# Performance work log

Hardware: AMD Instinct MI355X
Metric: run time of the kernel (lower is better)

The kernel has to match this reference:

```python
import jax, jax.numpy as jnp
import numpy as np

L, D, H = 4096, 1024, 16
HEAD_DIM = D // H
SCALE = 1.0 / float(np.sqrt(HEAD_DIM))


def setup_inputs() -> dict:
    key = jax.random.key(0)
    kq, kk, kv = jax.random.split(key, 3)
    Q = jax.random.normal(kq, (L, D), dtype=jnp.float32)
    K = jax.random.normal(kk, (L, D), dtype=jnp.float32)
    V = jax.random.normal(kv, (L, D), dtype=jnp.float32)
    return {"Q": Q, "K": K, "V": V}


def reference(Q, K, V):
    # [L, D] -> [H, L, head_dim]; contiguous head slices of D (matches the
    # original per-head slicing Q[:, h*hd:(h+1)*hd]).
    q = Q.reshape(L, H, HEAD_DIM).transpose(1, 0, 2)
    k = K.reshape(L, H, HEAD_DIM).transpose(1, 0, 2)
    v = V.reshape(L, H, HEAD_DIM).transpose(1, 0, 2)
    # scores: [H, L, L]
    scores = jnp.einsum('hqd,hkd->hqk', q, k) * SCALE
    probs = jax.nn.softmax(scores, axis=-1)
    out = jnp.einsum('hqk,hkd->hqd', probs, v)  # [H, L, head_dim]
    # merge heads back to [L, D]
    return out.transpose(1, 0, 2).reshape(L, D)
```

## Files before the change

### kernel.cpp

```cpp
#include <hip/hip_runtime.h>
#include <hip/hip_bf16.h>

#define SEQ_L 4096
#define DIM_D 1024
#define NHEAD 16
#define HDIM  64
#define QBLK  64
#define KVB   128
#define NTILE (SEQ_L / KVB)
#define QSCALE 0.180336880f
#define NSHIFT -17.3123405f

typedef __attribute__((ext_vector_type(8))) short bf16x8;
typedef __attribute__((ext_vector_type(4))) short bf16x4;
typedef __attribute__((ext_vector_type(4))) float f32x4;

__device__ __forceinline__ short f2bf(float f) {
    union { float f; unsigned u; } x; x.f = f;
    unsigned r = x.u + 0x7fffu + ((x.u >> 16) & 1u);
    return (short)(r >> 16);
}

__device__ __forceinline__ float fast_exp2(float x) {
#if __has_builtin(__builtin_amdgcn_exp2f)
    return __builtin_amdgcn_exp2f(x);
#else
    return exp2f(x);
#endif
}

__device__ __forceinline__ bf16x4 pk4t(float p0, float p1, float p2, float p3) {
#if __has_builtin(__builtin_amdgcn_perm)
    union { float f; unsigned u; } a0, a1, a2, a3;
    a0.f = p0; a1.f = p1; a2.f = p2; a3.f = p3;
    union { unsigned u[2]; bf16x4 v; } cv;
    cv.u[0] = __builtin_amdgcn_perm(a1.u, a0.u, 0x07060302u);
    cv.u[1] = __builtin_amdgcn_perm(a3.u, a2.u, 0x07060302u);
    return cv.v;
#else
    const bf16x4 r = { f2bf(p0), f2bf(p1), f2bf(p2), f2bf(p3) };
    return r;
#endif
}

__device__ __forceinline__ void gl16(const void* g, void* l) {
    __builtin_amdgcn_global_load_lds(
        (const __attribute__((address_space(1))) unsigned int*)g,
        (__attribute__((address_space(3))) unsigned int*)l, 16, 0, 0);
}

__global__ void cvt_qk(const float* __restrict__ Q, const float* __restrict__ K,
                       short* __restrict__ Qb, short* __restrict__ Kb) {
    const size_t n8 = (size_t)SEQ_L * DIM_D / 8;
    size_t j = (size_t)blockIdx.x * blockDim.x + threadIdx.x;
    const float* src; short* dst; float sc;
    if (j < n8) { src = Q; dst = Qb; sc = QSCALE; }
    else        { src = K; dst = Kb; sc = 1.0f; j -= n8; }
    const float4 a = *(const float4*)(src + j*8);
    const float4 b = *(const float4*)(src + j*8 + 4);
    bf16x8 v;
    v[0]=f2bf(a.x*sc); v[1]=f2bf(a.y*sc); v[2]=f2bf(a.z*sc); v[3]=f2bf(a.w*sc);
    v[4]=f2bf(b.x*sc); v[5]=f2bf(b.y*sc); v[6]=f2bf(b.z*sc); v[7]=f2bf(b.w*sc);
    *(bf16x8*)(dst + j*8) = v;
}

__global__ void cvt_vT(const float* __restrict__ V, short* __restrict__ VT) {
    __shared__ short tile[64][136];
    const int t = threadIdx.x;
    const int kv0 = blockIdx.x * 128;
    const int h = blockIdx.y;
#pragma unroll
    for (int i = 0; i < 8; ++i) {
        const int idx = i*256 + t;
        const int row = idx >> 4, cg = idx & 15;
        const float4 v = *(const float4*)(V + (size_t)(kv0+row)*DIM_D + h*HDIM + cg*4);
        tile[cg*4+0][row] = f2bf(v.x);
        tile[cg*4+1][row] = f2bf(v.y);
        tile[cg*4+2][row] = f2bf(v.z);
        tile[cg*4+3][row] = f2bf(v.w);
    }
    __syncthreads();
#pragma unroll
    for (int i = 0; i < 4; ++i) {
        const int idx = i*256 + t;
        const int d = idx >> 4, cg = idx & 15;
        *(bf16x8*)(VT + ((size_t)h*HDIM + d)*SEQ_L + kv0 + cg*8) = *(const bf16x8*)&tile[d][cg*8];
    }
}

__launch_bounds__(256, 2)
__global__ void attn_split(const short* __restrict__ Qb, const short* __restrict__ Kb,
                           const short* __restrict__ VT, float* __restrict__ Og) {
    __shared__ union {
        struct { short K[KVB*64]; short V[8192]; } s;
        struct { float Ob0[64*68]; float Ob1[64*68]; float ls[4][64]; } r;
    } u;

    const int t = threadIdx.x;
    const int w = t >> 6, lane = t & 63;
    const int g = lane >> 4, c = lane & 15;
    const int c7 = c & 7;

    const int flat = blockIdx.x;
    const int f2 = (flat & 7) * 128 + (flat >> 3);
    const int h = f2 >> 6, qi = f2 & 63;
    const int qb = qi * QBLK, hc = h * HDIM;

    bf16x8 qa[4][2];
#pragma unroll
    for (int qt = 0; qt < 4; ++qt)
#pragma unroll
        for (int ds = 0; ds < 2; ++ds)
            qa[qt][ds] = *(const bf16x8*)&Qb[(size_t)(qb + qt*16 + c) * DIM_D + hc + ds*32 + g*8];

    f32x4 o[4][4], os[4];
#pragma unroll
    for (int qt = 0; qt < 4; ++qt) {
        os[qt] = (f32x4){0.f,0.f,0.f,0.f};
#pragma unroll
        for (int db = 0; db < 4; ++db) o[qt][db] = (f32x4){0.f,0.f,0.f,0.f};
    }
    const short oneb = (short)0x3F80;
    const bf16x8 ones8 = { oneb, oneb, oneb, oneb, oneb, oneb, oneb, oneb };

    int koff[4], vgo[4]; unsigned kdst[4], vdst[4];
#pragma unroll
    for (int i = 0; i < 4; ++i) {
        const int s = lane >> 3;
        const int jj = i*8 + s;
        const int kvp = ((jj & 15) >> 2)*8 + (jj >> 4)*4 + (jj & 3);
        koff[i] = (w*32 + kvp) * DIM_D + (((lane & 7) ^ s) * 8);
        kdst[i] = (unsigned)(w*32 + i*8) * 128;
        vgo[i]  = (i*16 + c) * SEQ_L + w*32 + g*8;
        vdst[i] = (unsigned)(w*4096 + i*1024);
    }

    const short* Kh  = Kb + hc;
    const short* VTh = VT + (size_t)h * HDIM * SEQ_L;

#pragma unroll
    for (int i = 0; i < 4; ++i) {
        gl16(Kh + koff[i], (char*)u.s.K + kdst[i]);
        gl16(VTh + vgo[i], (char*)u.s.V + vdst[i]);
    }

    for (int tile = 0; tile < NTILE; ++tile) {
        asm volatile("s_waitcnt vmcnt(0)" ::: "memory");
        __builtin_amdgcn_sched_barrier(0);

        bf16x8 kf[2][2];
#pragma unroll
        for (int ktl = 0; ktl < 2; ++ktl)
#pragma unroll
            for (int ds = 0; ds < 2; ++ds)
                kf[ktl][ds] = *(const bf16x8*)&u.s.K[(w*32 + ktl*16 + c)*64 + (((ds*4 + g) ^ c7) * 8)];

        bf16x8 vv8[4];
#pragma unroll
        for (int db = 0; db < 4; ++db)
            vv8[db] = *(const bf16x8*)&u.s.V[w*2048 + db*512 + (g*16 + c)*8];

        asm volatile("s_waitcnt lgkmcnt(0)" ::: "memory");
        __builtin_amdgcn_sched_barrier(0);

        if (tile + 1 < NTILE) {
            const short* Kt = Kh + (size_t)(tile + 1) * KVB * DIM_D;
            const short* Vt = VTh + (tile + 1) * KVB;
#pragma unroll
            for (int i = 0; i < 4; ++i) {
                gl16(Kt + koff[i], (char*)u.s.K + kdst[i]);
                gl16(Vt + vgo[i], (char*)u.s.V + vdst[i]);
            }
        }

        __builtin_amdgcn_s_setprio(1);
#pragma unroll
        for (int qt = 0; qt < 4; ++qt) {
            f32x4 a0 = (f32x4){NSHIFT, NSHIFT, NSHIFT, NSHIFT};
            f32x4 a1 = (f32x4){NSHIFT, NSHIFT, NSHIFT, NSHIFT};
            a0 = __builtin_amdgcn_mfma_f32_16x16x32_bf16(kf[0][0], qa[qt][0], a0, 0, 0, 0);
            a0 = __builtin_amdgcn_mfma_f32_16x16x32_bf16(kf[0][1], qa[qt][1], a0, 0, 0, 0);
            a1 = __builtin_amdgcn_mfma_f32_16x16x32_bf16(kf[1][0], qa[qt][0], a1, 0, 0, 0);
            a1 = __builtin_amdgcn_mfma_f32_16x16x32_bf16(kf[1][1], qa[qt][1], a1, 0, 0, 0);

            const float p00 = fast_exp2(a0[0]), p01 = fast_exp2(a0[1]);
            const float p02 = fast_exp2(a0[2]), p03 = fast_exp2(a0[3]);
            const float p10 = fast_exp2(a1[0]), p11 = fast_exp2(a1[1]);
            const float p12 = fast_exp2(a1[2]), p13 = fast_exp2(a1[3]);
            const bf16x4 pl = pk4t(p00, p01, p02, p03);
            const bf16x4 ph = pk4t(p10, p11, p12, p13);
            const bf16x8 pb8 = __builtin_shufflevector(pl, ph, 0, 1, 2, 3, 4, 5, 6, 7);

            os[qt] = __builtin_amdgcn_mfma_f32_16x16x32_bf16(ones8, pb8, os[qt], 0, 0, 0);
#pragma unroll
            for (int db = 0; db < 4; ++db)
                o[qt][db] = __builtin_amdgcn_mfma_f32_16x16x32_bf16(vv8[db], pb8, o[qt][db], 0, 0, 0);
        }
        __builtin_amdgcn_s_setprio(0);
    }

    __syncthreads();
    if (lane < 16) {
#pragma unroll
        for (int qt = 0; qt < 4; ++qt) u.r.ls[w][qt*16 + c] = os[qt][0];
    }
    if (w == 0) {
#pragma unroll
        for (int qt = 0; qt < 4; ++qt)
#pragma unroll
            for (int db = 0; db < 4; ++db)
                *(f32x4*)&u.r.Ob0[(qt*16 + c)*68 + db*16 + 4*g] = o[qt][db];
    } else if (w == 1) {
#pragma unroll
        for (int qt = 0; qt < 4; ++qt)
#pragma unroll
            for (int db = 0; db < 4; ++db)
                *(f32x4*)&u.r.Ob1[(qt*16 + c)*68 + db*16 + 4*g] = o[qt][db];
    }
    __syncthreads();
    if (w == 2) {
#pragma unroll
        for (int qt = 0; qt < 4; ++qt)
#pragma unroll
            for (int db = 0; db < 4; ++db) {
                f32x4* p = (f32x4*)&u.r.Ob0[(qt*16 + c)*68 + db*16 + 4*g];
                f32x4 s = *p;
#pragma unroll
                for (int r = 0; r < 4; ++r) s[r] += o[qt][db][r];
                *p = s;
            }
    } else if (w == 3) {
#pragma unroll
        for (int qt = 0; qt < 4; ++qt)
#pragma unroll
            for (int db = 0; db < 4; ++db) {
                f32x4* p = (f32x4*)&u.r.Ob1[(qt*16 + c)*68 + db*16 + 4*g];
                f32x4 s = *p;
#pragma unroll
                for (int r = 0; r < 4; ++r) s[r] += o[qt][db][r];
                *p = s;
            }
    }
    __syncthreads();

    {
        const int row = w*16 + (lane >> 2);
        const int cq = lane & 3;
        const float lt = u.r.ls[0][row] + u.r.ls[1][row] + u.r.ls[2][row] + u.r.ls[3][row];
        const float inv = 1.0f / lt;
        float* op = Og + (size_t)(qb + row) * DIM_D + hc + cq*16;
#pragma unroll
        for (int i = 0; i < 4; ++i) {
            float4 v;
            v.x = (u.r.Ob0[row*68 + cq*16 + i*4 + 0] + u.r.Ob1[row*68 + cq*16 + i*4 + 0]) * inv;
            v.y = (u.r.Ob0[row*68 + cq*16 + i*4 + 1] + u.r.Ob1[row*68 + cq*16 + i*4 + 1]) * inv;
            v.z = (u.r.Ob0[row*68 + cq*16 + i*4 + 2] + u.r.Ob1[row*68 + cq*16 + i*4 + 2]) * inv;
            v.w = (u.r.Ob0[row*68 + cq*16 + i*4 + 3] + u.r.Ob1[row*68 + cq*16 + i*4 + 3]) * inv;
            *(float4*)(op + i*4) = v;
        }
    }
}

#define LDKF 72
__global__ void attn_fwd_fallback(const float* __restrict__ Qg, const float* __restrict__ Kg,
                                  const float* __restrict__ Vg, float* __restrict__ Og) {
    __shared__ short Klds[64 * LDKF];
    __shared__ short Vt[HDIM * LDKF];
    __shared__ short Plds[4 * 16 * LDKF];

    const int t = threadIdx.x;
    const int w = t >> 6, lane = t & 63;
    const int g = lane >> 4, c = lane & 15;
    const int qb = blockIdx.x * 64;
    const int h = blockIdx.y, hc = h * HDIM;

    bf16x8 qa[2];
    {
        const int qrow = qb + w * 16 + c;
        const float* qp = Qg + (size_t)qrow * DIM_D + hc + g * 8;
#pragma unroll
        for (int db = 0; db < 2; ++db) {
            bf16x8 a2;
#pragma unroll
            for (int j = 0; j < 8; ++j) a2[j] = f2bf(qp[db * 32 + j] * 0.125f);
            qa[db] = a2;
        }
    }
    float m[4], lsum[4];
    f32x4 o[4];
#pragma unroll
    for (int r = 0; r < 4; ++r) { m[r] = -1e30f; lsum[r] = 0.f; }
#pragma unroll
    for (int db = 0; db < 4; ++db) o[db] = (f32x4){0.f,0.f,0.f,0.f};
    const int tr = t >> 4, tc = t & 15;

    for (int kv0 = 0; kv0 < SEQ_L; kv0 += 64) {
#pragma unroll
        for (int i = 0; i < 4; ++i) {
            const int kv = tr + i * 16;
            const float4 kf4 = *(const float4*)(Kg + (size_t)(kv0 + kv) * DIM_D + hc + tc * 4);
            short4 ks; ks.x = f2bf(kf4.x); ks.y = f2bf(kf4.y); ks.z = f2bf(kf4.z); ks.w = f2bf(kf4.w);
            *(short4*)&Klds[kv * LDKF + tc * 4] = ks;
            const float4 vf4 = *(const float4*)(Vg + (size_t)(kv0 + kv) * DIM_D + hc + tc * 4);
            Vt[(tc*4+0) * LDKF + kv] = f2bf(vf4.x);
            Vt[(tc*4+1) * LDKF + kv] = f2bf(vf4.y);
            Vt[(tc*4+2) * LDKF + kv] = f2bf(vf4.z);
            Vt[(tc*4+3) * LDKF + kv] = f2bf(vf4.w);
        }
        __syncthreads();
        f32x4 acc[4];
#pragma unroll
        for (int kt = 0; kt < 4; ++kt) {
            f32x4 a2 = (f32x4){0.f,0.f,0.f,0.f};
#pragma unroll
            for (int db = 0; db < 2; ++db) {
                bf16x8 kb = *(const bf16x8*)&Klds[(kt*16 + c) * LDKF + db*32 + g*8];
                a2 = __builtin_amdgcn_mfma_f32_16x16x32_bf16(qa[db], kb, a2, 0, 0, 0);
            }
            acc[kt] = a2;
        }
        float tmax[4];
#pragma unroll
        for (int r = 0; r < 4; ++r)
            tmax[r] = fmaxf(fmaxf(acc[0][r], acc[1][r]), fmaxf(acc[2][r], acc[3][r]));
#pragma unroll
        for (int mask = 1; mask < 16; mask <<= 1)
#pragma unroll
            for (int r = 0; r < 4; ++r) tmax[r] = fmaxf(tmax[r], __shfl_xor(tmax[r], mask));
        float alpha[4], ps[4];
#pragma unroll
        for (int r = 0; r < 4; ++r) {
            const float mn = fmaxf(m[r], tmax[r]);
            alpha[r] = __expf(m[r] - mn); m[r] = mn; ps[r] = 0.f;
        }
#pragma unroll
        for (int kt = 0; kt < 4; ++kt)
#pragma unroll
            for (int r = 0; r < 4; ++r) {
                const float p = __expf(acc[kt][r] - m[r]);
                ps[r] += p;
                Plds[(w*16 + g*4 + r) * LDKF + kt*16 + c] = f2bf(p);
            }
#pragma unroll
        for (int mask = 1; mask < 16; mask <<= 1)
#pragma unroll
            for (int r = 0; r < 4; ++r) ps[r] += __shfl_xor(ps[r], mask);
#pragma unroll
        for (int r = 0; r < 4; ++r) lsum[r] = lsum[r] * alpha[r] + ps[r];
#pragma unroll
        for (int db = 0; db < 4; ++db)
#pragma unroll
            for (int r = 0; r < 4; ++r) o[db][r] *= alpha[r];
#pragma unroll
        for (int db = 0; db < 4; ++db)
#pragma unroll
            for (int kb = 0; kb < 2; ++kb) {
                bf16x8 pa = *(const bf16x8*)&Plds[(w*16 + c) * LDKF + kb*32 + g*8];
                bf16x8 vb = *(const bf16x8*)&Vt[(db*16 + c) * LDKF + kb*32 + g*8];
                o[db] = __builtin_amdgcn_mfma_f32_16x16x32_bf16(pa, vb, o[db], 0, 0, 0);
            }
        __syncthreads();
    }
#pragma unroll
    for (int r = 0; r < 4; ++r) {
        const float inv = 1.0f / lsum[r];
        const int qrow = qb + w*16 + g*4 + r;
        float* op = Og + (size_t)qrow * DIM_D + hc;
#pragma unroll
        for (int db = 0; db < 4; ++db) op[db*16 + c] = o[db][r] * inv;
    }
}

extern "C" void kernel_launch(void* const* d_in, const int* in_sizes, int n_in,
                              void* d_out, int out_size, void* d_ws, size_t ws_size,
                              hipStream_t stream) {
    (void)in_sizes; (void)n_in; (void)out_size;
    const float* Q = (const float*)d_in[0];
    const float* K = (const float*)d_in[1];
    const float* V = (const float*)d_in[2];
    float* O = (float*)d_out;

    const size_t n = (size_t)SEQ_L * DIM_D;
    const size_t need = 3 * n * sizeof(short);
    if (ws_size >= need) {
        short* Qb = (short*)d_ws;
        short* Kb = Qb + n;
        short* VT = Qb + 2 * n;
        hipLaunchKernelGGL(cvt_qk, dim3(2 * n / 8 / 256), dim3(256), 0, stream, Q, K, Qb, Kb);
        hipLaunchKernelGGL(cvt_vT, dim3(SEQ_L / 128, NHEAD), dim3(256), 0, stream, V, VT);
        hipLaunchKernelGGL(attn_split, dim3(1024), dim3(256), 0, stream, Qb, Kb, VT, O);
    } else {
        hipLaunchKernelGGL(attn_fwd_fallback, dim3(SEQ_L / 64, NHEAD), dim3(256), 0, stream, Q, K, V, O);
    }
}
```

Measured before the change: 106.4 us.

## Halve query block to 32 rows, raise occupancy, compute row sums with VALU

Shrinks the per-block query tile from 64 to 32 rows, which doubles the grid to 2048 blocks and raises the launch-bounds occupancy target from 2 to 3 blocks per CU. It also replaces the ones-vector MFMA used for softmax denominators with scalar adds plus cross-lane shuffles, and remaps the epilogue so each thread writes 8 output floats. The goal is more parallelism and latency hiding plus fewer MFMA issues per tile. The cost is that each K/V tile now serves half as many queries, which doubles global K/V traffic and the staging work per query.

```diff
diff --git a/kernel.cpp b/kernel.cpp
--- a/kernel.cpp
+++ b/kernel.cpp
@@ -5,7 +5,7 @@
 #define DIM_D 1024
 #define NHEAD 16
 #define HDIM  64
-#define QBLK  64
+#define QBLK  32
 #define KVB   128
 #define NTILE (SEQ_L / KVB)
 #define QSCALE 0.180336880f
@@ -88,12 +88,12 @@
     }
 }
 
-__launch_bounds__(256, 2)
+__launch_bounds__(256, 3)
 __global__ void attn_split(const short* __restrict__ Qb, const short* __restrict__ Kb,
                            const short* __restrict__ VT, float* __restrict__ Og) {
     __shared__ union {
         struct { short K[KVB*64]; short V[8192]; } s;
-        struct { float Ob0[64*68]; float Ob1[64*68]; float ls[4][64]; } r;
+        struct { float Ob0[32*68]; float Ob1[32*68]; float ls[4][32]; } r;
     } u;
 
     const int t = threadIdx.x;
@@ -102,26 +102,25 @@
     const int c7 = c & 7;
 
     const int flat = blockIdx.x;
-    const int f2 = (flat & 7) * 128 + (flat >> 3);
-    const int h = f2 >> 6, qi = f2 & 63;
+    const int f2 = (flat & 7) * 256 + (flat >> 3);
+    const int h = f2 >> 7, qi = f2 & 127;
     const int qb = qi * QBLK, hc = h * HDIM;
 
-    bf16x8 qa[4][2];
-#pragma unroll
-    for (int qt = 0; qt < 4; ++qt)
+    bf16x8 qa[2][2];
+#pragma unroll
+    for (int qt = 0; qt < 2; ++qt)
 #pragma unroll
         for (int ds = 0; ds < 2; ++ds)
             qa[qt][ds] = *(const bf16x8*)&Qb[(size_t)(qb + qt*16 + c) * DIM_D + hc + ds*32 + g*8];
 
-    f32x4 o[4][4], os[4];
-#pragma unroll
-    for (int qt = 0; qt < 4; ++qt) {
-        os[qt] = (f32x4){0.f,0.f,0.f,0.f};
+    f32x4 o[2][4];
+    float psum[2];
+#pragma unroll
+    for (int qt = 0; qt < 2; ++qt) {
+        psum[qt] = 0.f;
 #pragma unroll
         for (int db = 0; db < 4; ++db) o[qt][db] = (f32x4){0.f,0.f,0.f,0.f};
     }
-    const short oneb = (short)0x3F80;
-    const bf16x8 ones8 = { oneb, oneb, oneb, oneb, oneb, oneb, oneb, oneb };
 
     int koff[4], vgo[4]; unsigned kdst[4], vdst[4];
 #pragma unroll
@@ -175,7 +174,7 @@
 
         __builtin_amdgcn_s_setprio(1);
 #pragma unroll
-        for (int qt = 0; qt < 4; ++qt) {
+        for (int qt = 0; qt < 2; ++qt) {
             f32x4 a0 = (f32x4){NSHIFT, NSHIFT, NSHIFT, NSHIFT};
             f32x4 a1 = (f32x4){NSHIFT, NSHIFT, NSHIFT, NSHIFT};
             a0 = __builtin_amdgcn_mfma_f32_16x16x32_bf16(kf[0][0], qa[qt][0], a0, 0, 0, 0);
@@ -187,11 +186,11 @@
             const float p02 = fast_exp2(a0[2]), p03 = fast_exp2(a0[3]);
             const float p10 = fast_exp2(a1[0]), p11 = fast_exp2(a1[1]);
             const float p12 = fast_exp2(a1[2]), p13 = fast_exp2(a1[3]);
+            psum[qt] += ((p00 + p01) + (p02 + p03)) + ((p10 + p11) + (p12 + p13));
             const bf16x4 pl = pk4t(p00, p01, p02, p03);
             const bf16x4 ph = pk4t(p10, p11, p12, p13);
             const bf16x8 pb8 = __builtin_shufflevector(pl, ph, 0, 1, 2, 3, 4, 5, 6, 7);
 
-            os[qt] = __builtin_amdgcn_mfma_f32_16x16x32_bf16(ones8, pb8, os[qt], 0, 0, 0);
 #pragma unroll
             for (int db = 0; db < 4; ++db)
                 o[qt][db] = __builtin_amdgcn_mfma_f32_16x16x32_bf16(vv8[db], pb8, o[qt][db], 0, 0, 0);
@@ -199,20 +198,25 @@
         __builtin_amdgcn_s_setprio(0);
     }
 
+#pragma unroll
+    for (int qt = 0; qt < 2; ++qt) {
+        psum[qt] += __shfl_xor(psum[qt], 16);
+        psum[qt] += __shfl_xor(psum[qt], 32);
+    }
     __syncthreads();
     if (lane < 16) {
-#pragma unroll
-        for (int qt = 0; qt < 4; ++qt) u.r.ls[w][qt*16 + c] = os[qt][0];
+        u.r.ls[w][c]      = psum[0];
+        u.r.ls[w][16 + c] = psum[1];
     }
     if (w == 0) {
 #pragma unroll
-        for (int qt = 0; qt < 4; ++qt)
+        for (int qt = 0; qt < 2; ++qt)
 #pragma unroll
             for (int db = 0; db < 4; ++db)
                 *(f32x4*)&u.r.Ob0[(qt*16 + c)*68 + db*16 + 4*g] = o[qt][db];
     } else if (w == 1) {
 #pragma unroll
-        for (int qt = 0; qt < 4; ++qt)
+        for (int qt = 0; qt < 2; ++qt)
 #pragma unroll
             for (int db = 0; db < 4; ++db)
                 *(f32x4*)&u.r.Ob1[(qt*16 + c)*68 + db*16 + 4*g] = o[qt][db];
@@ -220,7 +224,7 @@
     __syncthreads();
     if (w == 2) {
 #pragma unroll
-        for (int qt = 0; qt < 4; ++qt)
+        for (int qt = 0; qt < 2; ++qt)
 #pragma unroll
             for (int db = 0; db < 4; ++db) {
                 f32x4* p = (f32x4*)&u.r.Ob0[(qt*16 + c)*68 + db*16 + 4*g];
@@ -231,7 +235,7 @@
             }
     } else if (w == 3) {
 #pragma unroll
-        for (int qt = 0; qt < 4; ++qt)
+        for (int qt = 0; qt < 2; ++qt)
 #pragma unroll
             for (int db = 0; db < 4; ++db) {
                 f32x4* p = (f32x4*)&u.r.Ob1[(qt*16 + c)*68 + db*16 + 4*g];
@@ -244,20 +248,23 @@
     __syncthreads();
 
     {
-        const int row = w*16 + (lane >> 2);
-        const int cq = lane & 3;
+        const int row = t >> 3;
+        const int j8 = t & 7;
         const float lt = u.r.ls[0][row] + u.r.ls[1][row] + u.r.ls[2][row] + u.r.ls[3][row];
         const float inv = 1.0f / lt;
-        float* op = Og + (size_t)(qb + row) * DIM_D + hc + cq*16;
-#pragma unroll
-        for (int i = 0; i < 4; ++i) {
-            float4 v;
-            v.x = (u.r.Ob0[row*68 + cq*16 + i*4 + 0] + u.r.Ob1[row*68 + cq*16 + i*4 + 0]) * inv;
-            v.y = (u.r.Ob0[row*68 + cq*16 + i*4 + 1] + u.r.Ob1[row*68 + cq*16 + i*4 + 1]) * inv;
-            v.z = (u.r.Ob0[row*68 + cq*16 + i*4 + 2] + u.r.Ob1[row*68 + cq*16 + i*4 + 2]) * inv;
-            v.w = (u.r.Ob0[row*68 + cq*16 + i*4 + 3] + u.r.Ob1[row*68 + cq*16 + i*4 + 3]) * inv;
-            *(float4*)(op + i*4) = v;
-        }
+        const int base = row*68 + j8*8;
+        float* op = Og + (size_t)(qb + row) * DIM_D + hc + j8*8;
+        float4 v0, v1;
+        v0.x = (u.r.Ob0[base + 0] + u.r.Ob1[base + 0]) * inv;
+        v0.y = (u.r.Ob0[base + 1] + u.r.Ob1[base + 1]) * inv;
+        v0.z = (u.r.Ob0[base + 2] + u.r.Ob1[base + 2]) * inv;
+        v0.w = (u.r.Ob0[base + 3] + u.r.Ob1[base + 3]) * inv;
+        v1.x = (u.r.Ob0[base + 4] + u.r.Ob1[base + 4]) * inv;
+        v1.y = (u.r.Ob0[base + 5] + u.r.Ob1[base + 5]) * inv;
+        v1.z = (u.r.Ob0[base + 6] + u.r.Ob1[base + 6]) * inv;
+        v1.w = (u.r.Ob0[base + 7] + u.r.Ob1[base + 7]) * inv;
+        *(float4*)op = v0;
+        *(float4*)(op + 4) = v1;
     }
 }
 
@@ -388,7 +395,7 @@
         short* VT = Qb + 2 * n;
         hipLaunchKernelGGL(cvt_qk, dim3(2 * n / 8 / 256), dim3(256), 0, stream, Q, K, Qb, Kb);
         hipLaunchKernelGGL(cvt_vT, dim3(SEQ_L / 128, NHEAD), dim3(256), 0, stream, V, VT);
-        hipLaunchKernelGGL(attn_split, dim3(1024), dim3(256), 0, stream, Qb, Kb, VT, O);
+        hipLaunchKernelGGL(attn_split, dim3(SEQ_L / QBLK * NHEAD), dim3(256), 0, stream, Qb, Kb, VT, O);
     } else {
         hipLaunchKernelGGL(attn_fwd_fallback, dim3(SEQ_L / 64, NHEAD), dim3(256), 0, stream, Q, K, V, O);
     }
```

New measurement: 170.2 us. +60.0%, slower.
